# Kernel tuning notes

Measured on AMD Instinct MI355X. Metric: run time of the kernel, lower is better.

The kernel has to match this reference:

```python
import jax, jax.numpy as jnp
import numpy as np

N = 50000      # nodes
E = 800000     # edges (avg degree 16)
F = 128        # num_features
H = 128        # hidden_channels
C = 16         # num_classes
KEEP = 0.5     # dropout keep prob


def setup_inputs() -> dict:
    key = jax.random.key(0)
    ks = jax.random.split(key, 7)
    x = jax.random.normal(ks[0], (N, F), dtype=jnp.float32)
    edge_index = jax.random.randint(ks[1], (2, E), 0, N, dtype=jnp.int64)
    W1 = jax.random.normal(ks[2], (F, H), dtype=jnp.float32) / np.float32(np.sqrt(F))
    b1 = jnp.zeros((H,), dtype=jnp.float32)
    W2 = jax.random.normal(ks[3], (H, C), dtype=jnp.float32) / np.float32(np.sqrt(H))
    b2 = jnp.zeros((C,), dtype=jnp.float32)
    # deterministic dropout mask (train-mode dropout, prob=0.5), pre-scaled by 1/keep
    dropout_mask = (jax.random.uniform(ks[4], (N, H)) < KEEP).astype(jnp.float32) / np.float32(KEEP)
    return {"x": x, "edge_index": edge_index, "W1": W1, "b1": b1,
            "W2": W2, "b2": b2, "dropout_mask": dropout_mask}


def _gather_mean(h, src, dst, n_nodes):
    # irregular gather (h[src]) + segment scatter-add at dst, then mean by in-degree
    agg = jax.ops.segment_sum(h[src], dst, num_segments=n_nodes)  # [N, c]
    deg = jax.ops.segment_sum(jnp.ones_like(dst, dtype=h.dtype), dst, num_segments=n_nodes)
    return agg / jnp.maximum(deg, 1.0)[:, None]


def reference(x, edge_index, W1, b1, W2, b2, dropout_mask):
    src, dst = edge_index[0], edge_index[1]
    # linmaps1: 0th->1st order broadcast; identity for singleton reference domains
    h = _gather_mean(x, src, dst, N)          # ConvolutionalLayer_1P #1: gather
    h = h @ W1 + b1                           # linear transform
    h = jax.nn.relu(h)
    h = h * dropout_mask                      # Dropout(prob=0.5)
    h = _gather_mean(h, src, dst, N)          # ConvolutionalLayer_1P #2: gather
    out = h @ W2 + b2
    # linmaps0: 1st->0th order reduce; identity for singleton domains
    return out
```

## Files before the change

### kernel.cpp

```cpp
#include <hip/hip_runtime.h>

#define NNODES 50000
#define NEDGES 800000
#define FDIM 128
#define HDIM 128
#define CDIM 16

#define NBUCK 256
#define BCAP 6144

typedef __attribute__((ext_vector_type(8))) short bf16x8;
typedef __attribute__((ext_vector_type(4))) float f32x4;

__device__ __forceinline__ ushort f32_to_bf16_rne(float f) {
  unsigned u = __float_as_uint(f);
  unsigned rounded = u + 0x7fffu + ((u >> 16) & 1u);
  return (ushort)(rounded >> 16);
}
__device__ __forceinline__ float bf_lo(unsigned u) { return __uint_as_float(u << 16); }
__device__ __forceinline__ float bf_hi(unsigned u) { return __uint_as_float(u & 0xffff0000u); }

__global__ void k_prep(const float* __restrict__ x, ushort* __restrict__ xh,
                       const float* __restrict__ W1, ushort* __restrict__ W1T,
                       const float* __restrict__ W2, ushort* __restrict__ W2T,
                       int* __restrict__ gcur) {
  int t = blockIdx.x * blockDim.x + threadIdx.x;
  if (t < 1600000) {
    float4 v = *reinterpret_cast<const float4*>(&x[t * 4]);
    ushort4 o;
    o.x = f32_to_bf16_rne(v.x);
    o.y = f32_to_bf16_rne(v.y);
    o.z = f32_to_bf16_rne(v.z);
    o.w = f32_to_bf16_rne(v.w);
    *reinterpret_cast<ushort4*>(&xh[t * 4]) = o;
    return;
  }
  t -= 1600000;
  if (t < 16384) {
    int c = t >> 7, k = t & 127;
    W1T[c * 128 + k] = f32_to_bf16_rne(W1[k * 128 + c]);
    return;
  }
  t -= 16384;
  if (t < 2048) {
    int c = t >> 7, k = t & 127;
    W2T[c * 128 + k] = f32_to_bf16_rne(W2[k * 16 + c]);
    return;
  }
  t -= 2048;
  if (t < NBUCK) gcur[t] = t * BCAP;
}

__global__ __launch_bounds__(256) void k_binA(
    const int* __restrict__ src, const int* __restrict__ dst,
    int* __restrict__ gcur, unsigned* __restrict__ ebuf) {
  __shared__ int cnt[NBUCK];
  __shared__ int base[NBUCK];
  int tid = threadIdx.x;
  int e0 = blockIdx.x * 2048;
  cnt[tid] = 0;
  __syncthreads();
  int sv[8], dv[8];
  #pragma unroll
  for (int i = 0; i < 8; ++i) {
    int e = e0 + i * 256 + tid;
    if (e < NEDGES) {
      sv[i] = src[e];
      dv[i] = dst[e];
      atomicAdd(&cnt[dv[i] >> 8], 1);
    } else {
      dv[i] = -1;
    }
  }
  __syncthreads();
  base[tid] = atomicAdd(&gcur[tid], cnt[tid]);
  cnt[tid] = 0;
  __syncthreads();
  #pragma unroll
  for (int i = 0; i < 8; ++i) {
    if (dv[i] >= 0) {
      int b = dv[i] >> 8;
      int pos = base[b] + atomicAdd(&cnt[b], 1);
      if (pos < (b + 1) * BCAP)
        ebuf[pos] = ((unsigned)(dv[i] & 255) << 16) | (unsigned)sv[i];
    }
  }
}

__global__ __launch_bounds__(256) void k_binB(
    const int* __restrict__ gcur, const unsigned* __restrict__ ebuf,
    int* __restrict__ deg, int* __restrict__ offs, ushort* __restrict__ ssrc) {
  __shared__ int s[NBUCK];
  __shared__ int doff[NBUCK];
  __shared__ int dcur[NBUCK];
  int tid = threadIdx.x;
  int b = blockIdx.x;

  int c = gcur[tid] - tid * BCAP;
  if (c > BCAP) c = BCAP;
  s[tid] = c;
  for (int off = 1; off < 256; off <<= 1) {
    __syncthreads();
    int t = (tid >= off) ? s[tid - off] : 0;
    __syncthreads();
    s[tid] += t;
  }
  __syncthreads();
  int my_base = (b > 0) ? s[b - 1] : 0;
  int count = s[b] - my_base;

  dcur[tid] = 0;
  __syncthreads();
  const unsigned* eb = &ebuf[b * BCAP];
  for (int e = tid; e < count; e += 256) {
    atomicAdd(&dcur[eb[e] >> 16], 1);
  }
  __syncthreads();
  int dn = dcur[tid];
  s[tid] = dn;
  for (int off = 1; off < 256; off <<= 1) {
    __syncthreads();
    int t = (tid >= off) ? s[tid - off] : 0;
    __syncthreads();
    s[tid] += t;
  }
  __syncthreads();
  doff[tid] = s[tid] - dn;
  int node = b * 256 + tid;
  if (node < NNODES) {
    deg[node] = dn;
    offs[node] = my_base + doff[tid];
  }
  dcur[tid] = 0;
  __syncthreads();

  for (int e = tid; e < count; e += 256) {
    unsigned v = eb[e];
    int loc = v >> 16;
    int pos = my_base + doff[loc] + atomicAdd(&dcur[loc], 1);
    ssrc[pos] = (ushort)(v & 0xffffu);
  }
}

__global__ __launch_bounds__(256) void k_spmm1(
    const ushort* __restrict__ xh, const int* __restrict__ offs,
    const int* __restrict__ deg, const ushort* __restrict__ ssrc,
    ushort* __restrict__ aggh) {
  int tid = threadIdx.x;
  int grp = tid >> 4;
  int l16 = tid & 15;
  int n = blockIdx.x * 16 + grp;
  if (n >= NNODES) return;
  int start = offs[n];
  int d = deg[n];
  const ushort* base = xh + l16 * 8;
  float a0[8] = {0,0,0,0,0,0,0,0};
  float a1[8] = {0,0,0,0,0,0,0,0};
  float a2[8] = {0,0,0,0,0,0,0,0};
  float a3[8] = {0,0,0,0,0,0,0,0};
  int j = 0;
  for (; j + 3 < d; j += 4) {
    int s0 = ssrc[start + j + 0];
    int s1 = ssrc[start + j + 1];
    int s2 = ssrc[start + j + 2];
    int s3 = ssrc[start + j + 3];
    uint4 u0 = *reinterpret_cast<const uint4*>(base + s0 * FDIM);
    uint4 u1 = *reinterpret_cast<const uint4*>(base + s1 * FDIM);
    uint4 u2 = *reinterpret_cast<const uint4*>(base + s2 * FDIM);
    uint4 u3 = *reinterpret_cast<const uint4*>(base + s3 * FDIM);
    a0[0] += bf_lo(u0.x); a0[1] += bf_hi(u0.x); a0[2] += bf_lo(u0.y); a0[3] += bf_hi(u0.y);
    a0[4] += bf_lo(u0.z); a0[5] += bf_hi(u0.z); a0[6] += bf_lo(u0.w); a0[7] += bf_hi(u0.w);
    a1[0] += bf_lo(u1.x); a1[1] += bf_hi(u1.x); a1[2] += bf_lo(u1.y); a1[3] += bf_hi(u1.y);
    a1[4] += bf_lo(u1.z); a1[5] += bf_hi(u1.z); a1[6] += bf_lo(u1.w); a1[7] += bf_hi(u1.w);
    a2[0] += bf_lo(u2.x); a2[1] += bf_hi(u2.x); a2[2] += bf_lo(u2.y); a2[3] += bf_hi(u2.y);
    a2[4] += bf_lo(u2.z); a2[5] += bf_hi(u2.z); a2[6] += bf_lo(u2.w); a2[7] += bf_hi(u2.w);
    a3[0] += bf_lo(u3.x); a3[1] += bf_hi(u3.x); a3[2] += bf_lo(u3.y); a3[3] += bf_hi(u3.y);
    a3[4] += bf_lo(u3.z); a3[5] += bf_hi(u3.z); a3[6] += bf_lo(u3.w); a3[7] += bf_hi(u3.w);
  }
  for (; j < d; ++j) {
    int s0 = ssrc[start + j];
    uint4 u0 = *reinterpret_cast<const uint4*>(base + s0 * FDIM);
    a0[0] += bf_lo(u0.x); a0[1] += bf_hi(u0.x); a0[2] += bf_lo(u0.y); a0[3] += bf_hi(u0.y);
    a0[4] += bf_lo(u0.z); a0[5] += bf_hi(u0.z); a0[6] += bf_lo(u0.w); a0[7] += bf_hi(u0.w);
  }
  float inv = 1.0f / (float)(d > 0 ? d : 1);
  unsigned r[4];
  #pragma unroll
  for (int k = 0; k < 4; ++k) {
    float e0 = (a0[2 * k] + a1[2 * k] + a2[2 * k] + a3[2 * k]) * inv;
    float e1 = (a0[2 * k + 1] + a1[2 * k + 1] + a2[2 * k + 1] + a3[2 * k + 1]) * inv;
    r[k] = (unsigned)f32_to_bf16_rne(e0) | ((unsigned)f32_to_bf16_rne(e1) << 16);
  }
  uint4 o; o.x = r[0]; o.y = r[1]; o.z = r[2]; o.w = r[3];
  *reinterpret_cast<uint4*>(&aggh[(size_t)n * FDIM + l16 * 8]) = o;
}

#define HT_STRIDE 132
__global__ __launch_bounds__(256) void k_dense(
    const ushort* __restrict__ aggh, const ushort* __restrict__ W1T,
    const float* __restrict__ b1, const float* __restrict__ mask,
    const ushort* __restrict__ W2T, ushort* __restrict__ zh) {
  __shared__ ushort hT[4][16 * HT_STRIDE];
  int w = threadIdx.x >> 6;
  int lane = threadIdx.x & 63;
  int nw = blockIdx.x * 64 + w * 16;
  if (nw >= NNODES) return;
  int l15 = lane & 15, quad = lane >> 4;

  f32x4 acc[8];
  #pragma unroll
  for (int ct = 0; ct < 8; ++ct) acc[ct] = (f32x4){0.f, 0.f, 0.f, 0.f};

  const ushort* arow = &aggh[(size_t)(nw + l15) * 128 + quad * 8];
  #pragma unroll
  for (int kk = 0; kk < 4; ++kk) {
    bf16x8 a = *reinterpret_cast<const bf16x8*>(arow + kk * 32);
    #pragma unroll
    for (int ct = 0; ct < 8; ++ct) {
      bf16x8 b = *reinterpret_cast<const bf16x8*>(
          &W1T[(size_t)(ct * 16 + l15) * 128 + kk * 32 + quad * 8]);
      acc[ct] = __builtin_amdgcn_mfma_f32_16x16x32_bf16(a, b, acc[ct], 0, 0, 0);
    }
  }

  ushort* ht = hT[w];
  #pragma unroll
  for (int ct = 0; ct < 8; ++ct) {
    int col = ct * 16 + l15;
    float bb = b1[col];
    #pragma unroll
    for (int r = 0; r < 4; ++r) {
      int node = nw + quad * 4 + r;
      float v = acc[ct][r] + bb;
      v = v > 0.f ? v : 0.f;
      v *= mask[(size_t)node * 128 + col];
      ht[(quad * 4 + r) * HT_STRIDE + col] = f32_to_bf16_rne(v);
    }
  }

  f32x4 zacc = (f32x4){0.f, 0.f, 0.f, 0.f};
  #pragma unroll
  for (int kk = 0; kk < 4; ++kk) {
    const ushort* ap = &ht[l15 * HT_STRIDE + kk * 32 + quad * 8];
    ushort4 alo = *reinterpret_cast<const ushort4*>(ap);
    ushort4 ahi = *reinterpret_cast<const ushort4*>(ap + 4);
    bf16x8 a2 = (bf16x8){(short)alo.x, (short)alo.y, (short)alo.z, (short)alo.w,
                         (short)ahi.x, (short)ahi.y, (short)ahi.z, (short)ahi.w};
    bf16x8 b2 = *reinterpret_cast<const bf16x8*>(&W2T[l15 * 128 + kk * 32 + quad * 8]);
    zacc = __builtin_amdgcn_mfma_f32_16x16x32_bf16(a2, b2, zacc, 0, 0, 0);
  }
  #pragma unroll
  for (int r = 0; r < 4; ++r) {
    zh[(size_t)(nw + quad * 4 + r) * 16 + l15] = f32_to_bf16_rne(zacc[r]);
  }
}

__global__ void k_spmm2(const ushort* __restrict__ zh, const int* __restrict__ offs,
                        const int* __restrict__ deg, const ushort* __restrict__ ssrc,
                        const float* __restrict__ b2, float* __restrict__ out) {
  int tid = threadIdx.x;
  int nl = tid >> 4, c = tid & 15;
  int n = blockIdx.x * 8 + nl;
  if (n >= NNODES) return;
  int start = offs[n], d = deg[n];
  float a0 = 0.f, a1 = 0.f, a2 = 0.f, a3 = 0.f;
  int j = 0;
  for (; j + 3 < d; j += 4) {
    int s0 = ssrc[start + j + 0], s1 = ssrc[start + j + 1];
    int s2 = ssrc[start + j + 2], s3 = ssrc[start + j + 3];
    a0 += __uint_as_float((unsigned)zh[s0 * 16 + c] << 16);
    a1 += __uint_as_float((unsigned)zh[s1 * 16 + c] << 16);
    a2 += __uint_as_float((unsigned)zh[s2 * 16 + c] << 16);
    a3 += __uint_as_float((unsigned)zh[s3 * 16 + c] << 16);
  }
  for (; j < d; ++j) a0 += __uint_as_float((unsigned)zh[ssrc[start + j] * 16 + c] << 16);
  out[n * 16 + c] = (a0 + a1 + a2 + a3) / (float)(d > 0 ? d : 1) + b2[c];
}


extern "C" void kernel_launch(void* const* d_in, const int* in_sizes, int n_in,
                              void* d_out, int out_size, void* d_ws, size_t ws_size,
                              hipStream_t stream) {
  const float* x    = (const float*)d_in[0];
  const int*   ei   = (const int*)d_in[1];
  const float* W1   = (const float*)d_in[2];
  const float* b1   = (const float*)d_in[3];
  const float* W2   = (const float*)d_in[4];
  const float* b2   = (const float*)d_in[5];
  const float* mask = (const float*)d_in[6];
  float* out = (float*)d_out;

  const int* src = ei;
  const int* dst = ei + NEDGES;

  char* ws = (char*)d_ws;
  size_t o = 0;
  auto alloc = [&](size_t bytes) -> void* {
    void* p = ws + o;
    o += (bytes + 255) & ~(size_t)255;
    return p;
  };
  ushort*   aggh = (ushort*)alloc((size_t)NNODES * 128 * 2);
  ushort*   xh   = (ushort*)alloc((size_t)NNODES * 128 * 2);
  ushort*   zh   = (ushort*)alloc((size_t)NNODES * 16 * 2);
  ushort*   W1T  = (ushort*)alloc((size_t)128 * 128 * 2);
  ushort*   W2T  = (ushort*)alloc((size_t)16 * 128 * 2);
  int*      deg  = (int*)alloc((size_t)NNODES * 4);
  int*      offs = (int*)alloc((size_t)NNODES * 4);
  int*      gcur = (int*)alloc((size_t)NBUCK * 4);
  unsigned* ebuf = (unsigned*)alloc((size_t)NBUCK * BCAP * 4);
  ushort*   ssrc = (ushort*)alloc((size_t)NEDGES * 2);

  int prep_threads = 1600000 + 16384 + 2048 + NBUCK;

  k_prep<<<(prep_threads + 255) / 256, 256, 0, stream>>>(x, xh, W1, W1T, W2, W2T, gcur);
  k_binA<<<(NEDGES + 2047) / 2048, 256, 0, stream>>>(src, dst, gcur, ebuf);
  k_binB<<<NBUCK, 256, 0, stream>>>(gcur, ebuf, deg, offs, ssrc);
  k_spmm1<<<(NNODES + 15) / 16, 256, 0, stream>>>(xh, offs, deg, ssrc, aggh);
  k_dense<<<(NNODES + 63) / 64, 256, 0, stream>>>(aggh, W1T, b1, mask, W2T, zh);
  k_spmm2<<<(NNODES + 7) / 8, 128, 0, stream>>>(zh, offs, deg, ssrc, b2, out);
}
```

Before: 185.4 us.

## Fuse first aggregation with dense MLP via shared memory; merge prep and binning

New measurement: 186.6 us. About the same (+0.7%).

```diff
diff --git a/kernel.cpp b/kernel.cpp
--- a/kernel.cpp
+++ b/kernel.cpp
@@ -8,6 +8,7 @@
 
 #define NBUCK 256
 #define BCAP 6144
+#define NBA 391
 
 typedef __attribute__((ext_vector_type(8))) short bf16x8;
 typedef __attribute__((ext_vector_type(4))) float f32x4;
@@ -20,11 +21,47 @@
 __device__ __forceinline__ float bf_lo(unsigned u) { return __uint_as_float(u << 16); }
 __device__ __forceinline__ float bf_hi(unsigned u) { return __uint_as_float(u & 0xffff0000u); }
 
-__global__ void k_prep(const float* __restrict__ x, ushort* __restrict__ xh,
-                       const float* __restrict__ W1, ushort* __restrict__ W1T,
-                       const float* __restrict__ W2, ushort* __restrict__ W2T,
-                       int* __restrict__ gcur) {
-  int t = blockIdx.x * blockDim.x + threadIdx.x;
+__global__ __launch_bounds__(256) void k_prep_binA(
+    const int* __restrict__ src, const int* __restrict__ dst,
+    int* __restrict__ gcur, unsigned* __restrict__ ebuf,
+    const float* __restrict__ x, ushort* __restrict__ xh,
+    const float* __restrict__ W1, ushort* __restrict__ W1T,
+    const float* __restrict__ W2, ushort* __restrict__ W2T) {
+  __shared__ int cnt[NBUCK];
+  __shared__ int base[NBUCK];
+  int tid = threadIdx.x;
+  if (blockIdx.x < NBA) {
+    int e0 = blockIdx.x * 2048;
+    cnt[tid] = 0;
+    __syncthreads();
+    int sv[8], dv[8];
+    #pragma unroll
+    for (int i = 0; i < 8; ++i) {
+      int e = e0 + i * 256 + tid;
+      if (e < NEDGES) {
+        sv[i] = src[e];
+        dv[i] = dst[e];
+        atomicAdd(&cnt[dv[i] >> 8], 1);
+      } else {
+        dv[i] = -1;
+      }
+    }
+    __syncthreads();
+    base[tid] = atomicAdd(&gcur[tid], cnt[tid]);
+    cnt[tid] = 0;
+    __syncthreads();
+    #pragma unroll
+    for (int i = 0; i < 8; ++i) {
+      if (dv[i] >= 0) {
+        int b = dv[i] >> 8;
+        int pos = base[b] + atomicAdd(&cnt[b], 1);
+        if (pos < BCAP)
+          ebuf[b * BCAP + pos] = ((unsigned)(dv[i] & 255) << 16) | (unsigned)sv[i];
+      }
+    }
+    return;
+  }
+  int t = (blockIdx.x - NBA) * 256 + tid;
   if (t < 1600000) {
     float4 v = *reinterpret_cast<const float4*>(&x[t * 4]);
     ushort4 o;
@@ -45,45 +82,6 @@
   if (t < 2048) {
     int c = t >> 7, k = t & 127;
     W2T[c * 128 + k] = f32_to_bf16_rne(W2[k * 16 + c]);
-    return;
-  }
-  t -= 2048;
-  if (t < NBUCK) gcur[t] = t * BCAP;
-}
-
-__global__ __launch_bounds__(256) void k_binA(
-    const int* __restrict__ src, const int* __restrict__ dst,
-    int* __restrict__ gcur, unsigned* __restrict__ ebuf) {
-  __shared__ int cnt[NBUCK];
-  __shared__ int base[NBUCK];
-  int tid = threadIdx.x;
-  int e0 = blockIdx.x * 2048;
-  cnt[tid] = 0;
-  __syncthreads();
-  int sv[8], dv[8];
-  #pragma unroll
-  for (int i = 0; i < 8; ++i) {
-    int e = e0 + i * 256 + tid;
-    if (e < NEDGES) {
-      sv[i] = src[e];
-      dv[i] = dst[e];
-      atomicAdd(&cnt[dv[i] >> 8], 1);
-    } else {
-      dv[i] = -1;
-    }
-  }
-  __syncthreads();
-  base[tid] = atomicAdd(&gcur[tid], cnt[tid]);
-  cnt[tid] = 0;
-  __syncthreads();
-  #pragma unroll
-  for (int i = 0; i < 8; ++i) {
-    if (dv[i] >= 0) {
-      int b = dv[i] >> 8;
-      int pos = base[b] + atomicAdd(&cnt[b], 1);
-      if (pos < (b + 1) * BCAP)
-        ebuf[pos] = ((unsigned)(dv[i] & 255) << 16) | (unsigned)sv[i];
-    }
   }
 }
 
@@ -96,7 +94,7 @@
   int tid = threadIdx.x;
   int b = blockIdx.x;
 
-  int c = gcur[tid] - tid * BCAP;
+  int c = gcur[tid];
   if (c > BCAP) c = BCAP;
   s[tid] = c;
   for (int off = 1; off < 256; off <<= 1) {
@@ -142,76 +140,82 @@
   }
 }
 
-__global__ __launch_bounds__(256) void k_spmm1(
+#define AG_STRIDE 136
+#define HT_STRIDE 132
+__global__ __launch_bounds__(256) void k_spmm_dense(
     const ushort* __restrict__ xh, const int* __restrict__ offs,
     const int* __restrict__ deg, const ushort* __restrict__ ssrc,
-    ushort* __restrict__ aggh) {
+    const ushort* __restrict__ W1T, const float* __restrict__ b1,
+    const float* __restrict__ mask, const ushort* __restrict__ W2T,
+    ushort* __restrict__ zh) {
+  __shared__ ushort sAgg[64 * AG_STRIDE];
+  __shared__ ushort hT[4][16 * HT_STRIDE];
   int tid = threadIdx.x;
+  int nb = blockIdx.x * 64;
+
   int grp = tid >> 4;
   int l16 = tid & 15;
-  int n = blockIdx.x * 16 + grp;
-  if (n >= NNODES) return;
-  int start = offs[n];
-  int d = deg[n];
-  const ushort* base = xh + l16 * 8;
-  float a0[8] = {0,0,0,0,0,0,0,0};
-  float a1[8] = {0,0,0,0,0,0,0,0};
-  float a2[8] = {0,0,0,0,0,0,0,0};
-  float a3[8] = {0,0,0,0,0,0,0,0};
-  int j = 0;
-  for (; j + 3 < d; j += 4) {
-    int s0 = ssrc[start + j + 0];
-    int s1 = ssrc[start + j + 1];
-    int s2 = ssrc[start + j + 2];
-    int s3 = ssrc[start + j + 3];
-    uint4 u0 = *reinterpret_cast<const uint4*>(base + s0 * FDIM);
-    uint4 u1 = *reinterpret_cast<const uint4*>(base + s1 * FDIM);
-    uint4 u2 = *reinterpret_cast<const uint4*>(base + s2 * FDIM);
-    uint4 u3 = *reinterpret_cast<const uint4*>(base + s3 * FDIM);
-    a0[0] += bf_lo(u0.x); a0[1] += bf_hi(u0.x); a0[2] += bf_lo(u0.y); a0[3] += bf_hi(u0.y);
-    a0[4] += bf_lo(u0.z); a0[5] += bf_hi(u0.z); a0[6] += bf_lo(u0.w); a0[7] += bf_hi(u0.w);
-    a1[0] += bf_lo(u1.x); a1[1] += bf_hi(u1.x); a1[2] += bf_lo(u1.y); a1[3] += bf_hi(u1.y);
-    a1[4] += bf_lo(u1.z); a1[5] += bf_hi(u1.z); a1[6] += bf_lo(u1.w); a1[7] += bf_hi(u1.w);
-    a2[0] += bf_lo(u2.x); a2[1] += bf_hi(u2.x); a2[2] += bf_lo(u2.y); a2[3] += bf_hi(u2.y);
-    a2[4] += bf_lo(u2.z); a2[5] += bf_hi(u2.z); a2[6] += bf_lo(u2.w); a2[7] += bf_hi(u2.w);
-    a3[0] += bf_lo(u3.x); a3[1] += bf_hi(u3.x); a3[2] += bf_lo(u3.y); a3[3] += bf_hi(u3.y);
-    a3[4] += bf_lo(u3.z); a3[5] += bf_hi(u3.z); a3[6] += bf_lo(u3.w); a3[7] += bf_hi(u3.w);
-  }
-  for (; j < d; ++j) {
-    int s0 = ssrc[start + j];
-    uint4 u0 = *reinterpret_cast<const uint4*>(base + s0 * FDIM);
-    a0[0] += bf_lo(u0.x); a0[1] += bf_hi(u0.x); a0[2] += bf_lo(u0.y); a0[3] += bf_hi(u0.y);
-    a0[4] += bf_lo(u0.z); a0[5] += bf_hi(u0.z); a0[6] += bf_lo(u0.w); a0[7] += bf_hi(u0.w);
-  }
-  float inv = 1.0f / (float)(d > 0 ? d : 1);
-  unsigned r[4];
-  #pragma unroll
-  for (int k = 0; k < 4; ++k) {
-    float e0 = (a0[2 * k] + a1[2 * k] + a2[2 * k] + a3[2 * k]) * inv;
-    float e1 = (a0[2 * k + 1] + a1[2 * k + 1] + a2[2 * k + 1] + a3[2 * k + 1]) * inv;
-    r[k] = (unsigned)f32_to_bf16_rne(e0) | ((unsigned)f32_to_bf16_rne(e1) << 16);
-  }
-  uint4 o; o.x = r[0]; o.y = r[1]; o.z = r[2]; o.w = r[3];
-  *reinterpret_cast<uint4*>(&aggh[(size_t)n * FDIM + l16 * 8]) = o;
-}
-
-#define HT_STRIDE 132
-__global__ __launch_bounds__(256) void k_dense(
-    const ushort* __restrict__ aggh, const ushort* __restrict__ W1T,
-    const float* __restrict__ b1, const float* __restrict__ mask,
-    const ushort* __restrict__ W2T, ushort* __restrict__ zh) {
-  __shared__ ushort hT[4][16 * HT_STRIDE];
-  int w = threadIdx.x >> 6;
-  int lane = threadIdx.x & 63;
-  int nw = blockIdx.x * 64 + w * 16;
-  if (nw >= NNODES) return;
+  const ushort* gbase = xh + l16 * 8;
+  for (int i = 0; i < 4; ++i) {
+    int nl = grp * 4 + i;
+    int n = nb + nl;
+    uint4 o = make_uint4(0, 0, 0, 0);
+    if (n < NNODES) {
+      int start = offs[n];
+      int d = deg[n];
+      float a0[8] = {0,0,0,0,0,0,0,0};
+      float a1[8] = {0,0,0,0,0,0,0,0};
+      float a2[8] = {0,0,0,0,0,0,0,0};
+      float a3[8] = {0,0,0,0,0,0,0,0};
+      int j = 0;
+      for (; j + 3 < d; j += 4) {
+        int s0 = ssrc[start + j + 0];
+        int s1 = ssrc[start + j + 1];
+        int s2 = ssrc[start + j + 2];
+        int s3 = ssrc[start + j + 3];
+        uint4 u0 = *reinterpret_cast<const uint4*>(gbase + s0 * FDIM);
+        uint4 u1 = *reinterpret_cast<const uint4*>(gbase + s1 * FDIM);
+        uint4 u2 = *reinterpret_cast<const uint4*>(gbase + s2 * FDIM);
+        uint4 u3 = *reinterpret_cast<const uint4*>(gbase + s3 * FDIM);
+        a0[0] += bf_lo(u0.x); a0[1] += bf_hi(u0.x); a0[2] += bf_lo(u0.y); a0[3] += bf_hi(u0.y);
+        a0[4] += bf_lo(u0.z); a0[5] += bf_hi(u0.z); a0[6] += bf_lo(u0.w); a0[7] += bf_hi(u0.w);
+        a1[0] += bf_lo(u1.x); a1[1] += bf_hi(u1.x); a1[2] += bf_lo(u1.y); a1[3] += bf_hi(u1.y);
+        a1[4] += bf_lo(u1.z); a1[5] += bf_hi(u1.z); a1[6] += bf_lo(u1.w); a1[7] += bf_hi(u1.w);
+        a2[0] += bf_lo(u2.x); a2[1] += bf_hi(u2.x); a2[2] += bf_lo(u2.y); a2[3] += bf_hi(u2.y);
+        a2[4] += bf_lo(u2.z); a2[5] += bf_hi(u2.z); a2[6] += bf_lo(u2.w); a2[7] += bf_hi(u2.w);
+        a3[0] += bf_lo(u3.x); a3[1] += bf_hi(u3.x); a3[2] += bf_lo(u3.y); a3[3] += bf_hi(u3.y);
+        a3[4] += bf_lo(u3.z); a3[5] += bf_hi(u3.z); a3[6] += bf_lo(u3.w); a3[7] += bf_hi(u3.w);
+      }
+      for (; j < d; ++j) {
+        int s0 = ssrc[start + j];
+        uint4 u0 = *reinterpret_cast<const uint4*>(gbase + s0 * FDIM);
+        a0[0] += bf_lo(u0.x); a0[1] += bf_hi(u0.x); a0[2] += bf_lo(u0.y); a0[3] += bf_hi(u0.y);
+        a0[4] += bf_lo(u0.z); a0[5] += bf_hi(u0.z); a0[6] += bf_lo(u0.w); a0[7] += bf_hi(u0.w);
+      }
+      float inv = 1.0f / (float)(d > 0 ? d : 1);
+      unsigned r[4];
+      #pragma unroll
+      for (int k = 0; k < 4; ++k) {
+        float e0 = (a0[2 * k] + a1[2 * k] + a2[2 * k] + a3[2 * k]) * inv;
+        float e1 = (a0[2 * k + 1] + a1[2 * k + 1] + a2[2 * k + 1] + a3[2 * k + 1]) * inv;
+        r[k] = (unsigned)f32_to_bf16_rne(e0) | ((unsigned)f32_to_bf16_rne(e1) << 16);
+      }
+      o.x = r[0]; o.y = r[1]; o.z = r[2]; o.w = r[3];
+    }
+    *reinterpret_cast<uint4*>(&sAgg[nl * AG_STRIDE + l16 * 8]) = o;
+  }
+  __syncthreads();
+
+  int w = tid >> 6;
+  int lane = tid & 63;
   int l15 = lane & 15, quad = lane >> 4;
+  int nw = nb + w * 16;
 
   f32x4 acc[8];
   #pragma unroll
   for (int ct = 0; ct < 8; ++ct) acc[ct] = (f32x4){0.f, 0.f, 0.f, 0.f};
 
-  const ushort* arow = &aggh[(size_t)(nw + l15) * 128 + quad * 8];
+  const ushort* arow = &sAgg[(w * 16 + l15) * AG_STRIDE + quad * 8];
   #pragma unroll
   for (int kk = 0; kk < 4; ++kk) {
     bf16x8 a = *reinterpret_cast<const bf16x8*>(arow + kk * 32);
@@ -231,9 +235,12 @@
     #pragma unroll
     for (int r = 0; r < 4; ++r) {
       int node = nw + quad * 4 + r;
-      float v = acc[ct][r] + bb;
-      v = v > 0.f ? v : 0.f;
-      v *= mask[(size_t)node * 128 + col];
+      float v = 0.f;
+      if (node < NNODES) {
+        v = acc[ct][r] + bb;
+        v = v > 0.f ? v : 0.f;
+        v *= mask[(size_t)node * 128 + col];
+      }
       ht[(quad * 4 + r) * HT_STRIDE + col] = f32_to_bf16_rne(v);
     }
   }
@@ -251,7 +258,9 @@
   }
   #pragma unroll
   for (int r = 0; r < 4; ++r) {
-    zh[(size_t)(nw + quad * 4 + r) * 16 + l15] = f32_to_bf16_rne(zacc[r]);
+    int node = nw + quad * 4 + r;
+    if (node < NNODES)
+      zh[(size_t)node * 16 + l15] = f32_to_bf16_rne(zacc[r]);
   }
 }
 
@@ -300,7 +309,6 @@
     o += (bytes + 255) & ~(size_t)255;
     return p;
   };
-  ushort*   aggh = (ushort*)alloc((size_t)NNODES * 128 * 2);
   ushort*   xh   = (ushort*)alloc((size_t)NNODES * 128 * 2);
   ushort*   zh   = (ushort*)alloc((size_t)NNODES * 16 * 2);
   ushort*   W1T  = (ushort*)alloc((size_t)128 * 128 * 2);
@@ -311,12 +319,14 @@
   unsigned* ebuf = (unsigned*)alloc((size_t)NBUCK * BCAP * 4);
   ushort*   ssrc = (ushort*)alloc((size_t)NEDGES * 2);
 
-  int prep_threads = 1600000 + 16384 + 2048 + NBUCK;
-
-  k_prep<<<(prep_threads + 255) / 256, 256, 0, stream>>>(x, xh, W1, W1T, W2, W2T, gcur);
-  k_binA<<<(NEDGES + 2047) / 2048, 256, 0, stream>>>(src, dst, gcur, ebuf);
+  int prep_threads = 1600000 + 16384 + 2048;
+  int prep_blocks = (prep_threads + 255) / 256;
+
+  hipMemsetAsync(gcur, 0, NBUCK * sizeof(int), stream);
+  k_prep_binA<<<NBA + prep_blocks, 256, 0, stream>>>(src, dst, gcur, ebuf,
+                                                     x, xh, W1, W1T, W2, W2T);
   k_binB<<<NBUCK, 256, 0, stream>>>(gcur, ebuf, deg, offs, ssrc);
-  k_spmm1<<<(NNODES + 15) / 16, 256, 0, stream>>>(xh, offs, deg, ssrc, aggh);
-  k_dense<<<(NNODES + 63) / 64, 256, 0, stream>>>(aggh, W1T, b1, mask, W2T, zh);
+  k_spmm_dense<<<(NNODES + 63) / 64, 256, 0, stream>>>(xh, offs, deg, ssrc,
+                                                       W1T, b1, mask, W2T, zh);
   k_spmm2<<<(NNODES + 7) / 8, 128, 0, stream>>>(zh, offs, deg, ssrc, b2, out);
 }
```
